# Kernel tuning notes

Hardware: AMD Instinct MI355X
Metric: run time of the kernel (lower is better)

## Reference

```python
import jax, jax.numpy as jnp
import numpy as np


def setup_inputs() -> dict:
    key = jax.random.key(0)
    kq, kk, kv = jax.random.split(key, 3)
    B, Nq, Nk, d = 16, 4096, 4096, 128
    return {
        "query": jax.random.normal(kq, (B, Nq, d), dtype=jnp.float32),
        "key": jax.random.normal(kk, (B, Nk, d), dtype=jnp.float32),
        "value": jax.random.normal(kv, (B, Nk, d), dtype=jnp.float32),
    }


def reference(query, key, value):
    # weights = softmax(QK^T / sqrt(d)) with causal mask; dropout p=0.0 is identity
    d = key.shape[-1]
    scale = 1.0 / jnp.sqrt(jnp.asarray(d, dtype=query.dtype))
    scores = jnp.einsum("bqd,bkd->bqk", query, key) * scale  # [B, Nq, Nk]
    Nq, Nk = scores.shape[-2], scores.shape[-1]
    causal = jnp.tril(jnp.ones((Nq, Nk), dtype=bool))
    scores = jnp.where(causal, scores, jnp.asarray(-jnp.inf, dtype=scores.dtype))
    weights = jax.nn.softmax(scores, axis=-1)
    return jnp.einsum("bqk,bkv->bqv", weights, value)
```

## Files before the change

### kernel.cpp

```cpp
#include <hip/hip_runtime.h>
#include <stdint.h>


#define NB 16
#define NS 4096
#define DH 128
#define FRAG_U16 8192

typedef float          fx4  __attribute__((ext_vector_type(4)));
typedef uint32_t       ux4  __attribute__((ext_vector_type(4)));
typedef __bf16         bfv8 __attribute__((ext_vector_type(8)));

typedef const uint32_t __attribute__((address_space(1))) glob_u32;
typedef uint32_t       __attribute__((address_space(3))) lds_u32;

__device__ __forceinline__ fx4 mfma16(bfv8 a, bfv8 b, fx4 c) {
  return __builtin_amdgcn_mfma_f32_16x16x32_bf16(a, b, c, 0, 0, 0);
}

__global__ void __launch_bounds__(256) prepack_kernel(
    const float* __restrict__ K, const float* __restrict__ V,
    unsigned short* __restrict__ Kf, unsigned short* __restrict__ Vf) {
  __shared__ __align__(16) unsigned short tile[64][136];
  const int bid = blockIdx.x;
  const int b = bid >> 6, kvblk = bid & 63;
  const int kvb = kvblk << 6;
  const int tid = threadIdx.x;
  const size_t fbase = ((size_t)(b * 64 + kvblk)) * FRAG_U16;

  {
    const int tt = tid >> 6, lane = tid & 63;
    const int ln16 = lane & 15, g = lane >> 4;
    const float* kp = K + (((size_t)(b * NS + kvb + 16 * tt + ln16)) << 7) + 8 * g;
    unsigned short* op = Kf + fbase + tt * 2048 + lane * 8;
#pragma unroll
    for (int c = 0; c < 4; ++c) {
      fx4 a0 = *(const fx4*)(kp + 32 * c);
      fx4 a1 = *(const fx4*)(kp + 32 * c + 4);
      bfv8 t;
#pragma unroll
      for (int j = 0; j < 4; ++j) {
        t[j]     = (__bf16)a0[j];
        t[j + 4] = (__bf16)a1[j];
      }
      *(ux4*)(op + c * 512) = __builtin_bit_cast(ux4, t);
    }
  }

  {
    const int r = tid >> 2, cq = tid & 3;
    const float* vp = V + (((size_t)(b * NS + kvb + r)) << 7) + 32 * cq;
#pragma unroll
    for (int h = 0; h < 4; ++h) {
      fx4 f0 = *(const fx4*)(vp + 8 * h);
      fx4 f1 = *(const fx4*)(vp + 8 * h + 4);
      bfv8 t;
#pragma unroll
      for (int j = 0; j < 4; ++j) {
        t[j]     = (__bf16)f0[j];
        t[j + 4] = (__bf16)f1[j];
      }
      *(ux4*)&tile[r][32 * cq + 8 * h] = __builtin_bit_cast(ux4, t);
    }
  }
  __syncthreads();
  {
    const int dt = tid >> 5, c = (tid >> 4) & 1, ln16 = tid & 15;
    const int d = 16 * dt + ln16;
    unsigned short* op = Vf + fbase + dt * 1024 + c * 512 + ln16 * 8;
#pragma unroll
    for (int g = 0; g < 4; ++g) {
      unsigned short e[8];
#pragma unroll
      for (int j = 0; j < 4; ++j) {
        e[j]     = tile[32 * c + 4 * g + j][d];
        e[j + 4] = tile[32 * c + 16 + 4 * g + j][d];
      }
      *(ux4*)(op + g * 128) = *(const ux4*)e;
    }
  }
}

__global__ void __launch_bounds__(256, 2) attn_kernel(
    const float* __restrict__ Q, const unsigned short* __restrict__ Kf,
    const unsigned short* __restrict__ Vf, float* __restrict__ O) {
  __shared__ __align__(16) unsigned char sm[65536];

  const int bid  = blockIdx.x;
  const int half = bid >> 8;
  const int i    = bid & 255;
  const int b    = i & 15;
  const int qi   = i >> 4;
  const int blkq = half ? qi : 31 - qi;
  const int qb   = blkq << 7;
  const int tid  = threadIdx.x;
  const int w    = tid >> 6;
  const int lane = tid & 63;
  const int g    = lane >> 4;
  const int ln16 = lane & 15;
  const int qw   = qb + 32 * w;

  const float SCALE = 0.12753102f;

  bfv8 qf[2][4];
#pragma unroll
  for (int qt = 0; qt < 2; ++qt) {
#pragma unroll
    for (int c = 0; c < 4; ++c) {
      const float* qp = Q + (((size_t)(b * NS + qw + qt * 16 + ln16)) << 7) + 32 * c + 8 * g;
      fx4 a0 = *(const fx4*)qp;
      fx4 a1 = *(const fx4*)(qp + 4);
      bfv8 t;
#pragma unroll
      for (int j = 0; j < 4; ++j) {
        t[j]     = (__bf16)(a0[j] * SCALE);
        t[j + 4] = (__bf16)(a1[j] * SCALE);
      }
      qf[qt][c] = t;
    }
  }

  const fx4 z4 = {0.f, 0.f, 0.f, 0.f};
  fx4 acc[2][8];
#pragma unroll
  for (int qt = 0; qt < 2; ++qt)
#pragma unroll
    for (int dt = 0; dt < 8; ++dt) acc[qt][dt] = z4;
  float mrun[2] = {-1e30f, -1e30f};
  float lsum[2] = {0.f, 0.f};

  const int nkv  = 2 * blkq + 2;
  const int nkvw = ((qw + 31) >> 6) + 1;

  const unsigned short* kfb = Kf + ((size_t)b * 64) * FRAG_U16;
  const unsigned short* vfb = Vf + ((size_t)b * 64) * FRAG_U16;

#define STAGE(jb, bufo)                                                        \
  do {                                                                         \
    const unsigned char* gk = (const unsigned char*)(kfb + (size_t)(jb)*FRAG_U16); \
    const unsigned char* gv = (const unsigned char*)(vfb + (size_t)(jb)*FRAG_U16); \
    _Pragma("unroll")                                                          \
    for (int ii = 0; ii < 4; ++ii) {                                           \
      const int off = ii * 4096 + w * 1024;                                    \
      __builtin_amdgcn_global_load_lds((glob_u32*)(gk + off + lane * 16),      \
                                       (lds_u32*)(sm + (bufo) + off), 16, 0, 0); \
      __builtin_amdgcn_global_load_lds((glob_u32*)(gv + off + lane * 16),      \
                                       (lds_u32*)(sm + (bufo) + 16384 + off), 16, 0, 0); \
    }                                                                          \
  } while (0)

  STAGE(0, 0);
  asm volatile("s_waitcnt vmcnt(0)" ::: "memory");
  __builtin_amdgcn_s_barrier();
  asm volatile("" ::: "memory");

  int cur = 0;
  for (int jb = 0; jb < nkv; ++jb) {
    if (jb + 1 < nkv) STAGE(jb + 1, (cur ^ 1) * 32768);

    if (jb < nkvw) {
      const unsigned char* kb = sm + cur * 32768;
      const unsigned char* vb = kb + 16384;

      fx4 s[2][4];
#pragma unroll
      for (int tt = 0; tt < 4; ++tt) { s[0][tt] = z4; s[1][tt] = z4; }
      __builtin_amdgcn_s_setprio(1);
#pragma unroll
      for (int tt = 0; tt < 4; ++tt) {
#pragma unroll
        for (int c = 0; c < 4; ++c) {
          bfv8 kfr = *(const bfv8*)(kb + tt * 4096 + c * 1024 + lane * 16);
          s[0][tt] = mfma16(kfr, qf[0][c], s[0][tt]);
          s[1][tt] = mfma16(kfr, qf[1][c], s[1][tt]);
        }
      }
      __builtin_amdgcn_s_setprio(0);

      bfv8 vfr[8][2];
#pragma unroll
      for (int dt = 0; dt < 8; ++dt)
#pragma unroll
        for (int c = 0; c < 2; ++c)
          vfr[dt][c] = *(const bfv8*)(vb + dt * 2048 + c * 1024 + lane * 16);

      const int kvb = jb << 6;
      if (kvb + 63 > qw) {
#pragma unroll
        for (int qt = 0; qt < 2; ++qt) {
          const int qrow = qw + qt * 16 + ln16;
#pragma unroll
          for (int tt = 0; tt < 4; ++tt)
#pragma unroll
            for (int r = 0; r < 4; ++r) {
              int kvpos = kvb + 16 * tt + 4 * g + r;
              if (kvpos > qrow) s[qt][tt][r] = -1e30f;
            }
        }
      }

      bfv8 pb[2][2];
#pragma unroll
      for (int qt = 0; qt < 2; ++qt) {
        fx4 m4 = __builtin_elementwise_max(
            __builtin_elementwise_max(s[qt][0], s[qt][1]),
            __builtin_elementwise_max(s[qt][2], s[qt][3]));
        float pm = fmaxf(fmaxf(m4[0], m4[1]), fmaxf(m4[2], m4[3]));
        pm = fmaxf(pm, __shfl_xor(pm, 16));
        pm = fmaxf(pm, __shfl_xor(pm, 32));
        float mq = mrun[qt];
        if (__any(pm > mq + 8.0f)) {
          float mn = fmaxf(mq, pm);
          float f  = __builtin_amdgcn_exp2f(mq - mn);
          lsum[qt] *= f;
#pragma unroll
          for (int dt = 0; dt < 8; ++dt) acc[qt][dt] *= f;
          mrun[qt] = mn;
          mq = mn;
        }
#pragma unroll
        for (int tt = 0; tt < 4; ++tt)
#pragma unroll
          for (int r = 0; r < 4; ++r)
            s[qt][tt][r] = __builtin_amdgcn_exp2f(s[qt][tt][r] - mq);
        fx4 r4 = (s[qt][0] + s[qt][1]) + (s[qt][2] + s[qt][3]);
        float rs = (r4[0] + r4[1]) + (r4[2] + r4[3]);
        rs += __shfl_xor(rs, 16);
        rs += __shfl_xor(rs, 32);
        lsum[qt] += rs;
#pragma unroll
        for (int c = 0; c < 2; ++c) {
          bfv8 t;
#pragma unroll
          for (int j = 0; j < 4; ++j) {
            t[j]     = (__bf16)s[qt][2 * c][j];
            t[j + 4] = (__bf16)s[qt][2 * c + 1][j];
          }
          pb[qt][c] = t;
        }
      }

      __builtin_amdgcn_s_setprio(1);
#pragma unroll
      for (int dt = 0; dt < 8; ++dt) {
#pragma unroll
        for (int c = 0; c < 2; ++c) {
          acc[0][dt] = mfma16(vfr[dt][c], pb[0][c], acc[0][dt]);
          acc[1][dt] = mfma16(vfr[dt][c], pb[1][c], acc[1][dt]);
        }
      }
      __builtin_amdgcn_s_setprio(0);
    }

    asm volatile("s_waitcnt vmcnt(0)" ::: "memory");
    __builtin_amdgcn_s_barrier();
    asm volatile("" ::: "memory");
    cur ^= 1;
  }
#undef STAGE

#pragma unroll
  for (int qt = 0; qt < 2; ++qt) {
    float inv = 1.0f / lsum[qt];
    float* ob = O + (((size_t)(b * NS + qw + qt * 16 + ln16)) << 7) + 4 * g;
#pragma unroll
    for (int dt = 0; dt < 8; ++dt) {
      fx4 o4 = acc[qt][dt] * inv;
      *(fx4*)(ob + 16 * dt) = o4;
    }
  }
}

extern "C" void kernel_launch(void* const* d_in, const int* in_sizes, int n_in,
                              void* d_out, int out_size, void* d_ws, size_t ws_size,
                              hipStream_t stream) {
  (void)in_sizes; (void)n_in; (void)out_size; (void)ws_size;
  const float* Q = (const float*)d_in[0];
  const float* K = (const float*)d_in[1];
  const float* V = (const float*)d_in[2];
  float* O = (float*)d_out;

  unsigned short* Kf = (unsigned short*)d_ws;
  unsigned short* Vf = Kf + (size_t)NB * NS * DH;

  prepack_kernel<<<dim3(NB * 64), dim3(256), 0, stream>>>(K, V, Kf, Vf);
  attn_kernel<<<dim3(512), dim3(256), 0, stream>>>(Q, Kf, Vf, O);
}
```

Before: 130.2 us.

## Split long causal query tiles across two workgroups with a merge kernel

When workspace allows, the long query tiles (upper half) are split along the KV axis. One workgroup handles the first 32 KV blocks and writes unnormalised fp32 output. Another handles the remaining KV blocks, stores a bf16 partial, then goes on to process a short query tile. A new merge kernel combines the two partials using the saved row max and sum. The aim is to balance per-workgroup work under the causal mask, at the cost of an extra launch, extra global traffic, and bf16 rounding of one partial.

```diff
diff --git a/kernel.cpp b/kernel.cpp
--- a/kernel.cpp
+++ b/kernel.cpp
@@ -7,9 +7,11 @@
 #define DH 128
 #define FRAG_U16 8192
 
-typedef float          fx4  __attribute__((ext_vector_type(4)));
-typedef uint32_t       ux4  __attribute__((ext_vector_type(4)));
-typedef __bf16         bfv8 __attribute__((ext_vector_type(8)));
+typedef float          fx4   __attribute__((ext_vector_type(4)));
+typedef uint32_t       ux4   __attribute__((ext_vector_type(4)));
+typedef __bf16         bfv8  __attribute__((ext_vector_type(8)));
+typedef __bf16         bfv4  __attribute__((ext_vector_type(4)));
+typedef unsigned short u16x4 __attribute__((ext_vector_type(4)));
 
 typedef const uint32_t __attribute__((address_space(1))) glob_u32;
 typedef uint32_t       __attribute__((address_space(3))) lds_u32;
@@ -83,54 +85,35 @@
 
 __global__ void __launch_bounds__(256, 2) attn_kernel(
     const float* __restrict__ Q, const unsigned short* __restrict__ Kf,
-    const unsigned short* __restrict__ Vf, float* __restrict__ O) {
+    const unsigned short* __restrict__ Vf, float* __restrict__ O,
+    unsigned short* __restrict__ Pa, float* __restrict__ Ml, int split) {
   __shared__ __align__(16) unsigned char sm[65536];
 
-  const int bid  = blockIdx.x;
-  const int half = bid >> 8;
-  const int i    = bid & 255;
-  const int b    = i & 15;
-  const int qi   = i >> 4;
-  const int blkq = half ? qi : 31 - qi;
-  const int qb   = blkq << 7;
+  const int wid  = blockIdx.x;
   const int tid  = threadIdx.x;
   const int w    = tid >> 6;
   const int lane = tid & 63;
   const int g    = lane >> 4;
   const int ln16 = lane & 15;
-  const int qw   = qb + 32 * w;
+
+  int b, t, j0, nc, mode, two = 0, t2 = 0;
+  if (split) {
+    if (wid < 256) {
+      b = wid & 15; t = 16 + (wid >> 4); j0 = 0; nc = 32; mode = 1;
+    } else {
+      const int u = wid - 256, p = u >> 4;
+      b = u & 15; t = 31 - p; j0 = 32; nc = 32 - 2 * p; mode = 2;
+      two = 1; t2 = p;
+    }
+  } else {
+    const int half = wid >> 8, i = wid & 255;
+    b = i & 15;
+    const int qi = i >> 4;
+    t = half ? qi : 31 - qi; j0 = 0; nc = 2 * t + 2; mode = 0;
+  }
 
   const float SCALE = 0.12753102f;
-
-  bfv8 qf[2][4];
-#pragma unroll
-  for (int qt = 0; qt < 2; ++qt) {
-#pragma unroll
-    for (int c = 0; c < 4; ++c) {
-      const float* qp = Q + (((size_t)(b * NS + qw + qt * 16 + ln16)) << 7) + 32 * c + 8 * g;
-      fx4 a0 = *(const fx4*)qp;
-      fx4 a1 = *(const fx4*)(qp + 4);
-      bfv8 t;
-#pragma unroll
-      for (int j = 0; j < 4; ++j) {
-        t[j]     = (__bf16)(a0[j] * SCALE);
-        t[j + 4] = (__bf16)(a1[j] * SCALE);
-      }
-      qf[qt][c] = t;
-    }
-  }
-
   const fx4 z4 = {0.f, 0.f, 0.f, 0.f};
-  fx4 acc[2][8];
-#pragma unroll
-  for (int qt = 0; qt < 2; ++qt)
-#pragma unroll
-    for (int dt = 0; dt < 8; ++dt) acc[qt][dt] = z4;
-  float mrun[2] = {-1e30f, -1e30f};
-  float lsum[2] = {0.f, 0.f};
-
-  const int nkv  = 2 * blkq + 2;
-  const int nkvw = ((qw + 31) >> 6) + 1;
 
   const unsigned short* kfb = Kf + ((size_t)b * 64) * FRAG_U16;
   const unsigned short* vfb = Vf + ((size_t)b * 64) * FRAG_U16;
@@ -149,132 +132,233 @@
     }                                                                          \
   } while (0)
 
-  STAGE(0, 0);
-  asm volatile("s_waitcnt vmcnt(0)" ::: "memory");
-  __builtin_amdgcn_s_barrier();
-  asm volatile("" ::: "memory");
-
-  int cur = 0;
-  for (int jb = 0; jb < nkv; ++jb) {
-    if (jb + 1 < nkv) STAGE(jb + 1, (cur ^ 1) * 32768);
-
-    if (jb < nkvw) {
-      const unsigned char* kb = sm + cur * 32768;
-      const unsigned char* vb = kb + 16384;
-
-      fx4 s[2][4];
-#pragma unroll
-      for (int tt = 0; tt < 4; ++tt) { s[0][tt] = z4; s[1][tt] = z4; }
-      __builtin_amdgcn_s_setprio(1);
-#pragma unroll
-      for (int tt = 0; tt < 4; ++tt) {
-#pragma unroll
-        for (int c = 0; c < 4; ++c) {
-          bfv8 kfr = *(const bfv8*)(kb + tt * 4096 + c * 1024 + lane * 16);
-          s[0][tt] = mfma16(kfr, qf[0][c], s[0][tt]);
-          s[1][tt] = mfma16(kfr, qf[1][c], s[1][tt]);
-        }
-      }
-      __builtin_amdgcn_s_setprio(0);
-
-      bfv8 vfr[8][2];
-#pragma unroll
-      for (int dt = 0; dt < 8; ++dt)
-#pragma unroll
-        for (int c = 0; c < 2; ++c)
-          vfr[dt][c] = *(const bfv8*)(vb + dt * 2048 + c * 1024 + lane * 16);
-
-      const int kvb = jb << 6;
-      if (kvb + 63 > qw) {
-#pragma unroll
-        for (int qt = 0; qt < 2; ++qt) {
-          const int qrow = qw + qt * 16 + ln16;
-#pragma unroll
-          for (int tt = 0; tt < 4; ++tt)
-#pragma unroll
-            for (int r = 0; r < 4; ++r) {
-              int kvpos = kvb + 16 * tt + 4 * g + r;
-              if (kvpos > qrow) s[qt][tt][r] = -1e30f;
-            }
-        }
-      }
-
-      bfv8 pb[2][2];
-#pragma unroll
-      for (int qt = 0; qt < 2; ++qt) {
-        fx4 m4 = __builtin_elementwise_max(
-            __builtin_elementwise_max(s[qt][0], s[qt][1]),
-            __builtin_elementwise_max(s[qt][2], s[qt][3]));
-        float pm = fmaxf(fmaxf(m4[0], m4[1]), fmaxf(m4[2], m4[3]));
-        pm = fmaxf(pm, __shfl_xor(pm, 16));
-        pm = fmaxf(pm, __shfl_xor(pm, 32));
-        float mq = mrun[qt];
-        if (__any(pm > mq + 8.0f)) {
-          float mn = fmaxf(mq, pm);
-          float f  = __builtin_amdgcn_exp2f(mq - mn);
-          lsum[qt] *= f;
-#pragma unroll
-          for (int dt = 0; dt < 8; ++dt) acc[qt][dt] *= f;
-          mrun[qt] = mn;
-          mq = mn;
-        }
-#pragma unroll
-        for (int tt = 0; tt < 4; ++tt)
-#pragma unroll
-          for (int r = 0; r < 4; ++r)
-            s[qt][tt][r] = __builtin_amdgcn_exp2f(s[qt][tt][r] - mq);
-        fx4 r4 = (s[qt][0] + s[qt][1]) + (s[qt][2] + s[qt][3]);
-        float rs = (r4[0] + r4[1]) + (r4[2] + r4[3]);
-        rs += __shfl_xor(rs, 16);
-        rs += __shfl_xor(rs, 32);
-        lsum[qt] += rs;
-#pragma unroll
-        for (int c = 0; c < 2; ++c) {
-          bfv8 t;
-#pragma unroll
-          for (int j = 0; j < 4; ++j) {
-            t[j]     = (__bf16)s[qt][2 * c][j];
-            t[j + 4] = (__bf16)s[qt][2 * c + 1][j];
-          }
-          pb[qt][c] = t;
-        }
-      }
-
-      __builtin_amdgcn_s_setprio(1);
-#pragma unroll
-      for (int dt = 0; dt < 8; ++dt) {
-#pragma unroll
-        for (int c = 0; c < 2; ++c) {
-          acc[0][dt] = mfma16(vfr[dt][c], pb[0][c], acc[0][dt]);
-          acc[1][dt] = mfma16(vfr[dt][c], pb[1][c], acc[1][dt]);
-        }
-      }
-      __builtin_amdgcn_s_setprio(0);
-    }
-
+  for (;;) {
+    const int qb = t << 7;
+    const int qw = qb + 32 * w;
+
+    bfv8 qf[2][4];
+#pragma unroll
+    for (int qt = 0; qt < 2; ++qt) {
+#pragma unroll
+      for (int c = 0; c < 4; ++c) {
+        const float* qp = Q + (((size_t)(b * NS + qw + qt * 16 + ln16)) << 7) + 32 * c + 8 * g;
+        fx4 a0 = *(const fx4*)qp;
+        fx4 a1 = *(const fx4*)(qp + 4);
+        bfv8 tt_;
+#pragma unroll
+        for (int j = 0; j < 4; ++j) {
+          tt_[j]     = (__bf16)(a0[j] * SCALE);
+          tt_[j + 4] = (__bf16)(a1[j] * SCALE);
+        }
+        qf[qt][c] = tt_;
+      }
+    }
+
+    fx4 acc[2][8];
+#pragma unroll
+    for (int qt = 0; qt < 2; ++qt)
+#pragma unroll
+      for (int dt = 0; dt < 8; ++dt) acc[qt][dt] = z4;
+    float mrun[2] = {-1e30f, -1e30f};
+    float lsum[2] = {0.f, 0.f};
+
+    const int nkvw = ((qw + 31) >> 6) + 1;
+    const int jend = j0 + nc;
+
+    STAGE(j0, 0);
     asm volatile("s_waitcnt vmcnt(0)" ::: "memory");
     __builtin_amdgcn_s_barrier();
     asm volatile("" ::: "memory");
-    cur ^= 1;
+
+    int cur = 0;
+    for (int jb = j0; jb < jend; ++jb) {
+      if (jb + 1 < jend) STAGE(jb + 1, (cur ^ 1) * 32768);
+
+      if (jb < nkvw) {
+        const unsigned char* kb = sm + cur * 32768;
+        const unsigned char* vb = kb + 16384;
+
+        fx4 s[2][4];
+#pragma unroll
+        for (int tt = 0; tt < 4; ++tt) { s[0][tt] = z4; s[1][tt] = z4; }
+        __builtin_amdgcn_s_setprio(1);
+#pragma unroll
+        for (int tt = 0; tt < 4; ++tt) {
+#pragma unroll
+          for (int c = 0; c < 4; ++c) {
+            bfv8 kfr = *(const bfv8*)(kb + tt * 4096 + c * 1024 + lane * 16);
+            s[0][tt] = mfma16(kfr, qf[0][c], s[0][tt]);
+            s[1][tt] = mfma16(kfr, qf[1][c], s[1][tt]);
+          }
+        }
+        __builtin_amdgcn_s_setprio(0);
+
+        bfv8 vfr[8][2];
+#pragma unroll
+        for (int dt = 0; dt < 8; ++dt)
+#pragma unroll
+          for (int c = 0; c < 2; ++c)
+            vfr[dt][c] = *(const bfv8*)(vb + dt * 2048 + c * 1024 + lane * 16);
+
+        const int kvb = jb << 6;
+        if (kvb + 63 > qw) {
+#pragma unroll
+          for (int qt = 0; qt < 2; ++qt) {
+            const int qrow = qw + qt * 16 + ln16;
+#pragma unroll
+            for (int tt = 0; tt < 4; ++tt)
+#pragma unroll
+              for (int r = 0; r < 4; ++r) {
+                int kvpos = kvb + 16 * tt + 4 * g + r;
+                if (kvpos > qrow) s[qt][tt][r] = -1e30f;
+              }
+          }
+        }
+
+        bfv8 pb[2][2];
+#pragma unroll
+        for (int qt = 0; qt < 2; ++qt) {
+          fx4 m4 = __builtin_elementwise_max(
+              __builtin_elementwise_max(s[qt][0], s[qt][1]),
+              __builtin_elementwise_max(s[qt][2], s[qt][3]));
+          float pm = fmaxf(fmaxf(m4[0], m4[1]), fmaxf(m4[2], m4[3]));
+          pm = fmaxf(pm, __shfl_xor(pm, 16));
+          pm = fmaxf(pm, __shfl_xor(pm, 32));
+          float mq = mrun[qt];
+          if (__any(pm > mq + 8.0f)) {
+            float mn = fmaxf(mq, pm);
+            float f  = __builtin_amdgcn_exp2f(mq - mn);
+            lsum[qt] *= f;
+#pragma unroll
+            for (int dt = 0; dt < 8; ++dt) acc[qt][dt] *= f;
+            mrun[qt] = mn;
+            mq = mn;
+          }
+#pragma unroll
+          for (int tt = 0; tt < 4; ++tt)
+#pragma unroll
+            for (int r = 0; r < 4; ++r)
+              s[qt][tt][r] = __builtin_amdgcn_exp2f(s[qt][tt][r] - mq);
+          fx4 r4 = (s[qt][0] + s[qt][1]) + (s[qt][2] + s[qt][3]);
+          float rs = (r4[0] + r4[1]) + (r4[2] + r4[3]);
+          rs += __shfl_xor(rs, 16);
+          rs += __shfl_xor(rs, 32);
+          lsum[qt] += rs;
+#pragma unroll
+          for (int c = 0; c < 2; ++c) {
+            bfv8 tt_;
+#pragma unroll
+            for (int j = 0; j < 4; ++j) {
+              tt_[j]     = (__bf16)s[qt][2 * c][j];
+              tt_[j + 4] = (__bf16)s[qt][2 * c + 1][j];
+            }
+            pb[qt][c] = tt_;
+          }
+        }
+
+        __builtin_amdgcn_s_setprio(1);
+#pragma unroll
+        for (int dt = 0; dt < 8; ++dt) {
+#pragma unroll
+          for (int c = 0; c < 2; ++c) {
+            acc[0][dt] = mfma16(vfr[dt][c], pb[0][c], acc[0][dt]);
+            acc[1][dt] = mfma16(vfr[dt][c], pb[1][c], acc[1][dt]);
+          }
+        }
+        __builtin_amdgcn_s_setprio(0);
+      }
+
+      asm volatile("s_waitcnt vmcnt(0)" ::: "memory");
+      __builtin_amdgcn_s_barrier();
+      asm volatile("" ::: "memory");
+      cur ^= 1;
+    }
+
+    if (mode == 0) {
+#pragma unroll
+      for (int qt = 0; qt < 2; ++qt) {
+        float inv = 1.0f / lsum[qt];
+        float* ob = O + (((size_t)(b * NS + qw + qt * 16 + ln16)) << 7) + 4 * g;
+#pragma unroll
+        for (int dt = 0; dt < 8; ++dt) *(fx4*)(ob + 16 * dt) = acc[qt][dt] * inv;
+      }
+    } else {
+      if (mode == 1) {
+#pragma unroll
+        for (int qt = 0; qt < 2; ++qt) {
+          float* ob = O + (((size_t)(b * NS + qw + qt * 16 + ln16)) << 7) + 4 * g;
+#pragma unroll
+          for (int dt = 0; dt < 8; ++dt) *(fx4*)(ob + 16 * dt) = acc[qt][dt];
+        }
+      } else {
+#pragma unroll
+        for (int qt = 0; qt < 2; ++qt) {
+          const int row = 32 * w + 16 * qt + ln16;
+          unsigned short* pp =
+              Pa + (((size_t)((b * 16 + (t - 16)) * 128 + row)) << 7) + 4 * g;
+#pragma unroll
+          for (int dt = 0; dt < 8; ++dt) {
+            bfv4 t4;
+#pragma unroll
+            for (int j = 0; j < 4; ++j) t4[j] = (__bf16)acc[qt][dt][j];
+            *(u16x4*)(pp + 16 * dt) = __builtin_bit_cast(u16x4, t4);
+          }
+        }
+      }
+      if (g == 0) {
+        const int slot = mode - 1;
+        float* mlp = Ml + (size_t)(((b * 16 + (t - 16)) * 2 + slot) * 2) * 128;
+#pragma unroll
+        for (int qt = 0; qt < 2; ++qt) {
+          const int row = 32 * w + 16 * qt + ln16;
+          mlp[row]       = mrun[qt];
+          mlp[128 + row] = lsum[qt];
+        }
+      }
+    }
+
+    if (!two) break;
+    two = 0; t = t2; j0 = 0; nc = 2 * t2 + 2; mode = 0;
   }
 #undef STAGE
-
-#pragma unroll
-  for (int qt = 0; qt < 2; ++qt) {
-    float inv = 1.0f / lsum[qt];
-    float* ob = O + (((size_t)(b * NS + qw + qt * 16 + ln16)) << 7) + 4 * g;
-#pragma unroll
-    for (int dt = 0; dt < 8; ++dt) {
-      fx4 o4 = acc[qt][dt] * inv;
-      *(fx4*)(ob + 16 * dt) = o4;
-    }
-  }
+}
+
+__global__ void __launch_bounds__(256) merge_kernel(
+    float* __restrict__ O, const unsigned short* __restrict__ Pa,
+    const float* __restrict__ Ml) {
+  const int gid = blockIdx.x * 256 + threadIdx.x;
+  const int d4  = gid & 31;
+  const int rg  = gid >> 5;
+  const int b   = rg >> 11;
+  const int r2  = rg & 2047;
+  const int tt  = r2 >> 7;
+  const int row = r2 & 127;
+
+  const float* mlp = Ml + (size_t)((b * 16 + tt) * 4) * 128;
+  const float m1 = mlp[row],       l1 = mlp[128 + row];
+  const float m2 = mlp[256 + row], l2 = mlp[384 + row];
+  const float m  = fmaxf(m1, m2);
+  const float w1 = __builtin_amdgcn_exp2f(m1 - m);
+  const float w2 = __builtin_amdgcn_exp2f(m2 - m);
+
+  float* op = O + (((size_t)(b * NS + (16 + tt) * 128 + row)) << 7) + 4 * d4;
+  fx4 a1 = *(const fx4*)op;
+  const unsigned short* pp =
+      Pa + (((size_t)((b * 16 + tt) * 128 + row)) << 7) + 4 * d4;
+  bfv4 a2b = __builtin_bit_cast(bfv4, *(const u16x4*)pp);
+  fx4 a2;
+#pragma unroll
+  for (int j = 0; j < 4; ++j) a2[j] = (float)a2b[j];
+
+  const float inv = 1.0f / (w1 * l1 + w2 * l2);
+  fx4 o = (a1 * w1 + a2 * w2) * inv;
+  *(fx4*)op = o;
 }
 
 extern "C" void kernel_launch(void* const* d_in, const int* in_sizes, int n_in,
                               void* d_out, int out_size, void* d_ws, size_t ws_size,
                               hipStream_t stream) {
-  (void)in_sizes; (void)n_in; (void)out_size; (void)ws_size;
+  (void)in_sizes; (void)n_in; (void)out_size;
   const float* Q = (const float*)d_in[0];
   const float* K = (const float*)d_in[1];
   const float* V = (const float*)d_in[2];
@@ -282,7 +366,13 @@
 
   unsigned short* Kf = (unsigned short*)d_ws;
   unsigned short* Vf = Kf + (size_t)NB * NS * DH;
+  unsigned short* Pa = Vf + (size_t)NB * NS * DH;
+  float*          Ml = (float*)((char*)d_ws + 41943040);
+
+  const size_t NEED = 41943040 + 524288;
+  const int split = (ws_size >= NEED) ? 1 : 0;
 
   prepack_kernel<<<dim3(NB * 64), dim3(256), 0, stream>>>(K, V, Kf, Vf);
-  attn_kernel<<<dim3(512), dim3(256), 0, stream>>>(Q, Kf, Vf, O);
-}
+  attn_kernel<<<dim3(512), dim3(256), 0, stream>>>(Q, Kf, Vf, O, Pa, Ml, split);
+  if (split) merge_kernel<<<dim3(4096), dim3(256), 0, stream>>>(O, Pa, Ml);
+}
```

Measured after the change: 118.3 us. 9.1% less time.
